# Performance work log

Measured on AMD Instinct MI355X. Metric: run time of the kernel, lower is better.

Reference implementation:

```python
import jax, jax.numpy as jnp
import numpy as np

# layer dims of the hard-coded linear chain (torch Linear: y = x @ W.T + b)
_DIMS = [784, 69, 31, 10, 10, 10, 10, 10, 10, 10]


def setup_inputs() -> dict:
    key = jax.random.key(0)
    ks = jax.random.split(key, 1 + 2 * 9)
    inp = {"x": jax.random.normal(ks[0], (65536, 784), dtype=jnp.float32)}
    for i in range(9):
        fan_in, fan_out = _DIMS[i], _DIMS[i + 1]
        bound = 1.0 / np.sqrt(fan_in)
        inp[f"W{i}"] = jax.random.uniform(ks[1 + 2 * i], (fan_out, fan_in), dtype=jnp.float32, minval=-bound, maxval=bound)
        inp[f"b{i}"] = jax.random.uniform(ks[2 + 2 * i], (fan_out,), dtype=jnp.float32, minval=-bound, maxval=bound)
    return inp


def reference(x, W0, b0, W1, b1, W2, b2, W3, b3, W4, b4, W5, b5, W6, b6, W7, b7, W8, b8):
    Ws = [W0, W1, W2, W3, W4, W5, W6, W7, W8]
    bs = [b0, b1, b2, b3, b4, b5, b6, b7, b8]
    for W, b in zip(Ws, bs):
        x = x @ W.T + b  # [B, out]
    return x
```

## Files before the change

### kernel.cpp

```cpp
#include <hip/hip_runtime.h>


__global__ void prep_all(
    const float* __restrict__ W0,
    const float* __restrict__ W1, const float* __restrict__ b1,
    const float* __restrict__ W2, const float* __restrict__ b2,
    const float* __restrict__ W3, const float* __restrict__ b3,
    const float* __restrict__ W4, const float* __restrict__ b4,
    const float* __restrict__ W5, const float* __restrict__ b5,
    const float* __restrict__ W6, const float* __restrict__ b6,
    const float* __restrict__ W7, const float* __restrict__ b7,
    const float* __restrict__ W8, const float* __restrict__ b8,
    const float* __restrict__ b0,
    float* __restrict__ Wt2, float* __restrict__ beff)
{
    __shared__ float Sa[31 * 69], Sb[31 * 69];
    __shared__ float da[31], db[31];
    const int t = threadIdx.x;
    const int nt = blockDim.x;

    for (int i = t; i < 31 * 69; i += nt) Sa[i] = W1[i];
    for (int i = t; i < 31; i += nt) da[i] = b1[i];
    __syncthreads();

    for (int i = t; i < 10 * 69; i += nt) {
        int o = i / 69, c = i - o * 69;
        float s = 0.f;
        for (int k = 0; k < 31; k++) s += W2[o * 31 + k] * Sa[k * 69 + c];
        Sb[i] = s;
    }
    for (int i = t; i < 10; i += nt) {
        float s = b2[i];
        for (int k = 0; k < 31; k++) s += W2[i * 31 + k] * da[k];
        db[i] = s;
    }
    __syncthreads();

    const float* Wk[6] = { W3, W4, W5, W6, W7, W8 };
    const float* bk[6] = { b3, b4, b5, b6, b7, b8 };
    int src = 1;
    for (int st = 0; st < 6; st++) {
        const float* W = Wk[st];
        const float* bb = bk[st];
        float* S  = src ? Sb : Sa;
        float* D  = src ? Sa : Sb;
        float* dd = src ? db : da;
        float* dn = src ? da : db;
        for (int i = t; i < 10 * 69; i += nt) {
            int o = i / 69, c = i - o * 69;
            float s = 0.f;
            for (int k = 0; k < 10; k++) s += W[o * 10 + k] * S[k * 69 + c];
            D[i] = s;
        }
        for (int i = t; i < 10; i += nt) {
            float s = bb[i];
            for (int k = 0; k < 10; k++) s += W[i * 10 + k] * dd[k];
            dn[i] = s;
        }
        __syncthreads();
        src ^= 1;
    }

    float* S  = src ? Sb : Sa;
    float* dd = src ? db : da;

    if (blockIdx.x == 0) {
        for (int i = t; i < 10; i += nt) {
            float s = dd[i];
            for (int k = 0; k < 69; k++) s += S[i * 69 + k] * b0[k];
            beff[i] = s;
        }
    }

    int e = blockIdx.x * nt + t;
    if (e < 8800) {
        int j4 = e / 44, rem = e - j4 * 44;
        float val = 0.f;
        if (rem < 40) {
            int o = rem >> 2, k = rem & 3, j = j4 * 4 + k;
            if (j < 784) {
                for (int u = 0; u < 69; u++) val += S[o * 69 + u] * W0[u * 784 + j];
            }
        }
        Wt2[e] = val;
    }
}


__global__ __launch_bounds__(512, 4) void linear_main(
    const float* __restrict__ x, const float* __restrict__ Wt2,
    const float* __restrict__ beff, float* __restrict__ out)
{
    __shared__ float4 wlds[2200];
    const int t = threadIdx.x;
    const int s = t & 7;
    const long row0 = (long)blockIdx.x * 128 + (t >> 3);
    const float* xr0 = x + row0 * 784;
    const float* xr1 = xr0 + (long)64 * 784;

    {
        const float4* wg = (const float4*)Wt2;
        for (int i = t; i < 2200; i += 512) wlds[i] = wg[i];
    }

    float acc0[10], acc1[10];
#pragma unroll
    for (int o = 0; o < 10; o++) { acc0[o] = 0.f; acc1[o] = 0.f; }

    float4 xv0 = *(const float4*)(xr0 + s * 4);
    float4 xv1 = *(const float4*)(xr1 + s * 4);
    __syncthreads();

    for (int jb = 0; jb < 25; jb++) {
        float4 xc0 = xv0, xc1 = xv1;
        if (jb < 24) {
            int jn = (jb + 1) * 32 + s * 4;
            jn = jn > 780 ? 780 : jn;
            xv0 = *(const float4*)(xr0 + jn);
            xv1 = *(const float4*)(xr1 + jn);
        }
        const float4* wrow = &wlds[(jb * 8 + s) * 11];
#pragma unroll
        for (int o = 0; o < 10; o++) {
            float4 wv = wrow[o];
            acc0[o] = fmaf(xc0.x, wv.x, acc0[o]);
            acc0[o] = fmaf(xc0.y, wv.y, acc0[o]);
            acc0[o] = fmaf(xc0.z, wv.z, acc0[o]);
            acc0[o] = fmaf(xc0.w, wv.w, acc0[o]);
            acc1[o] = fmaf(xc1.x, wv.x, acc1[o]);
            acc1[o] = fmaf(xc1.y, wv.y, acc1[o]);
            acc1[o] = fmaf(xc1.z, wv.z, acc1[o]);
            acc1[o] = fmaf(xc1.w, wv.w, acc1[o]);
        }
    }

#pragma unroll
    for (int m = 1; m < 8; m <<= 1)
#pragma unroll
        for (int o = 0; o < 10; o++) {
            acc0[o] += __shfl_xor(acc0[o], m, 64);
            acc1[o] += __shfl_xor(acc1[o], m, 64);
        }

    if (s < 5) {
        float lo0 = 0.f, hi0 = 0.f, lo1 = 0.f, hi1 = 0.f;
#pragma unroll
        for (int o = 0; o < 5; o++) {
            if (s == o) {
                lo0 = acc0[2 * o]; hi0 = acc0[2 * o + 1];
                lo1 = acc1[2 * o]; hi1 = acc1[2 * o + 1];
            }
        }
        float be0 = beff[s * 2], be1 = beff[s * 2 + 1];
        *(float2*)(out + row0 * 10 + s * 2) = make_float2(lo0 + be0, hi0 + be1);
        *(float2*)(out + (row0 + 64) * 10 + s * 2) = make_float2(lo1 + be0, hi1 + be1);
    }
}

extern "C" void kernel_launch(void* const* d_in, const int* in_sizes, int n_in,
                              void* d_out, int out_size, void* d_ws, size_t ws_size,
                              hipStream_t stream) {
    const float* x  = (const float*)d_in[0];
    const float* W0 = (const float*)d_in[1];
    const float* b0 = (const float*)d_in[2];
    const float* W1 = (const float*)d_in[3];
    const float* b1 = (const float*)d_in[4];
    const float* W2 = (const float*)d_in[5];
    const float* b2 = (const float*)d_in[6];
    const float* W3 = (const float*)d_in[7];
    const float* b3 = (const float*)d_in[8];
    const float* W4 = (const float*)d_in[9];
    const float* b4 = (const float*)d_in[10];
    const float* W5 = (const float*)d_in[11];
    const float* b5 = (const float*)d_in[12];
    const float* W6 = (const float*)d_in[13];
    const float* b6 = (const float*)d_in[14];
    const float* W7 = (const float*)d_in[15];
    const float* b7 = (const float*)d_in[16];
    const float* W8 = (const float*)d_in[17];
    const float* b8 = (const float*)d_in[18];

    float* ws   = (float*)d_ws;
    float* Wt2  = ws;
    float* beff = ws + 8800;

    float* out = (float*)d_out;
    const int B = in_sizes[0] / 784;

    prep_all<<<18, 512, 0, stream>>>(W0, W1, b1, W2, b2, W3, b3, W4, b4,
                                     W5, b5, W6, b6, W7, b7, W8, b8,
                                     b0, Wt2, beff);
    linear_main<<<B / 128, 512, 0, stream>>>(x, Wt2, beff, out);
}
```

Before: 335.9 us.

## Fuse weight-chain collapse into main kernel, recomputing per block

Removes the separate prep kernel and its global workspace round-trip. Each block now collapses W1..W8 and the bias chain in shared memory, then builds the 784x10 effective weight matrix directly into LDS before streaming x. This removes one launch and one dependency gap, but every one of the 512 blocks redoes the prep work, which costs about 0.5M FMAs plus W0 reads per block. Shared memory use also grows, which may reduce occupancy below the launch-bounds target.

Measured after the change: 364.2 us. 1.08x slower.

```diff
diff --git a/kernel.cpp b/kernel.cpp
--- a/kernel.cpp
+++ b/kernel.cpp
@@ -1,8 +1,9 @@
 #include <hip/hip_runtime.h>
 
 
-__global__ void prep_all(
-    const float* __restrict__ W0,
+__global__ __launch_bounds__(512, 4) void fused_main(
+    const float* __restrict__ x,
+    const float* __restrict__ W0, const float* __restrict__ b0,
     const float* __restrict__ W1, const float* __restrict__ b1,
     const float* __restrict__ W2, const float* __restrict__ b2,
     const float* __restrict__ W3, const float* __restrict__ b3,
@@ -11,28 +12,37 @@
     const float* __restrict__ W6, const float* __restrict__ b6,
     const float* __restrict__ W7, const float* __restrict__ b7,
     const float* __restrict__ W8, const float* __restrict__ b8,
-    const float* __restrict__ b0,
-    float* __restrict__ Wt2, float* __restrict__ beff)
+    float* __restrict__ out)
 {
+    __shared__ float4 wlds[2200];
     __shared__ float Sa[31 * 69], Sb[31 * 69];
-    __shared__ float da[31], db[31];
+    __shared__ float da[31], db[31], be[10];
+
     const int t = threadIdx.x;
-    const int nt = blockDim.x;
+    const int sseg = t & 7;
+    const long row0 = (long)blockIdx.x * 128 + (t >> 3);
+    const float* xr0 = x + row0 * 784;
+    const float* xr1 = xr0 + (long)64 * 784;
 
-    for (int i = t; i < 31 * 69; i += nt) Sa[i] = W1[i];
-    for (int i = t; i < 31; i += nt) da[i] = b1[i];
+    float4 xv0 = *(const float4*)(xr0 + sseg * 4);
+    float4 xv1 = *(const float4*)(xr1 + sseg * 4);
+
+    for (int i = t; i < 2200; i += 512) wlds[i] = make_float4(0.f, 0.f, 0.f, 0.f);
+
+    for (int i = t; i < 31 * 69; i += 512) Sa[i] = W1[i];
+    for (int i = t; i < 31; i += 512) da[i] = b1[i];
     __syncthreads();
 
-    for (int i = t; i < 10 * 69; i += nt) {
+    for (int i = t; i < 10 * 69; i += 512) {
         int o = i / 69, c = i - o * 69;
-        float s = 0.f;
-        for (int k = 0; k < 31; k++) s += W2[o * 31 + k] * Sa[k * 69 + c];
-        Sb[i] = s;
+        float v = 0.f;
+        for (int k = 0; k < 31; k++) v += W2[o * 31 + k] * Sa[k * 69 + c];
+        Sb[i] = v;
     }
-    for (int i = t; i < 10; i += nt) {
-        float s = b2[i];
-        for (int k = 0; k < 31; k++) s += W2[i * 31 + k] * da[k];
-        db[i] = s;
+    for (int i = t; i < 10; i += 512) {
+        float v = b2[i];
+        for (int k = 0; k < 31; k++) v += W2[i * 31 + k] * da[k];
+        db[i] = v;
     }
     __syncthreads();
 
@@ -46,16 +56,16 @@
         float* D  = src ? Sa : Sb;
         float* dd = src ? db : da;
         float* dn = src ? da : db;
-        for (int i = t; i < 10 * 69; i += nt) {
+        for (int i = t; i < 10 * 69; i += 512) {
             int o = i / 69, c = i - o * 69;
-            float s = 0.f;
-            for (int k = 0; k < 10; k++) s += W[o * 10 + k] * S[k * 69 + c];
-            D[i] = s;
+            float v = 0.f;
+            for (int k = 0; k < 10; k++) v += W[o * 10 + k] * S[k * 69 + c];
+            D[i] = v;
         }
-        for (int i = t; i < 10; i += nt) {
-            float s = bb[i];
-            for (int k = 0; k < 10; k++) s += W[i * 10 + k] * dd[k];
-            dn[i] = s;
+        for (int i = t; i < 10; i += 512) {
+            float v = bb[i];
+            for (int k = 0; k < 10; k++) v += W[i * 10 + k] * dd[k];
+            dn[i] = v;
         }
         __syncthreads();
         src ^= 1;
@@ -64,62 +74,57 @@
     float* S  = src ? Sb : Sa;
     float* dd = src ? db : da;
 
-    if (blockIdx.x == 0) {
-        for (int i = t; i < 10; i += nt) {
-            float s = dd[i];
-            for (int k = 0; k < 69; k++) s += S[i * 69 + k] * b0[k];
-            beff[i] = s;
+    for (int i = t; i < 10; i += 512) {
+        float v = dd[i];
+        for (int k = 0; k < 69; k++) v += S[i * 69 + k] * b0[k];
+        be[i] = v;
+    }
+
+    {
+        float a0[10], a1[10];
+#pragma unroll
+        for (int o = 0; o < 10; o++) { a0[o] = 0.f; a1[o] = 0.f; }
+        const bool two = (t < 272);
+        for (int u = 0; u < 69; u++) {
+            float s8v[10];
+#pragma unroll
+            for (int o = 0; o < 10; o++) s8v[o] = S[o * 69 + u];
+            float w0 = W0[u * 784 + t];
+#pragma unroll
+            for (int o = 0; o < 10; o++) a0[o] = fmaf(s8v[o], w0, a0[o]);
+            if (two) {
+                float w1 = W0[u * 784 + t + 512];
+#pragma unroll
+                for (int o = 0; o < 10; o++) a1[o] = fmaf(s8v[o], w1, a1[o]);
+            }
+        }
+        float* wf = (float*)wlds;
+        const int j = t;
+#pragma unroll
+        for (int o = 0; o < 10; o++)
+            wf[(j >> 2) * 44 + o * 4 + (j & 3)] = a0[o];
+        if (two) {
+            const int j2 = t + 512;
+#pragma unroll
+            for (int o = 0; o < 10; o++)
+                wf[(j2 >> 2) * 44 + o * 4 + (j2 & 3)] = a1[o];
         }
     }
-
-    int e = blockIdx.x * nt + t;
-    if (e < 8800) {
-        int j4 = e / 44, rem = e - j4 * 44;
-        float val = 0.f;
-        if (rem < 40) {
-            int o = rem >> 2, k = rem & 3, j = j4 * 4 + k;
-            if (j < 784) {
-                for (int u = 0; u < 69; u++) val += S[o * 69 + u] * W0[u * 784 + j];
-            }
-        }
-        Wt2[e] = val;
-    }
-}
-
-
-__global__ __launch_bounds__(512, 4) void linear_main(
-    const float* __restrict__ x, const float* __restrict__ Wt2,
-    const float* __restrict__ beff, float* __restrict__ out)
-{
-    __shared__ float4 wlds[2200];
-    const int t = threadIdx.x;
-    const int s = t & 7;
-    const long row0 = (long)blockIdx.x * 128 + (t >> 3);
-    const float* xr0 = x + row0 * 784;
-    const float* xr1 = xr0 + (long)64 * 784;
-
-    {
-        const float4* wg = (const float4*)Wt2;
-        for (int i = t; i < 2200; i += 512) wlds[i] = wg[i];
-    }
+    __syncthreads();
 
     float acc0[10], acc1[10];
 #pragma unroll
     for (int o = 0; o < 10; o++) { acc0[o] = 0.f; acc1[o] = 0.f; }
 
-    float4 xv0 = *(const float4*)(xr0 + s * 4);
-    float4 xv1 = *(const float4*)(xr1 + s * 4);
-    __syncthreads();
-
     for (int jb = 0; jb < 25; jb++) {
         float4 xc0 = xv0, xc1 = xv1;
         if (jb < 24) {
-            int jn = (jb + 1) * 32 + s * 4;
+            int jn = (jb + 1) * 32 + sseg * 4;
             jn = jn > 780 ? 780 : jn;
             xv0 = *(const float4*)(xr0 + jn);
             xv1 = *(const float4*)(xr1 + jn);
         }
-        const float4* wrow = &wlds[(jb * 8 + s) * 11];
+        const float4* wrow = &wlds[(jb * 8 + sseg) * 11];
 #pragma unroll
         for (int o = 0; o < 10; o++) {
             float4 wv = wrow[o];
@@ -142,18 +147,18 @@
             acc1[o] += __shfl_xor(acc1[o], m, 64);
         }
 
-    if (s < 5) {
+    if (sseg < 5) {
         float lo0 = 0.f, hi0 = 0.f, lo1 = 0.f, hi1 = 0.f;
 #pragma unroll
         for (int o = 0; o < 5; o++) {
-            if (s == o) {
+            if (sseg == o) {
                 lo0 = acc0[2 * o]; hi0 = acc0[2 * o + 1];
                 lo1 = acc1[2 * o]; hi1 = acc1[2 * o + 1];
             }
         }
-        float be0 = beff[s * 2], be1 = beff[s * 2 + 1];
-        *(float2*)(out + row0 * 10 + s * 2) = make_float2(lo0 + be0, hi0 + be1);
-        *(float2*)(out + (row0 + 64) * 10 + s * 2) = make_float2(lo1 + be0, hi1 + be1);
+        float be0 = be[sseg * 2], be1 = be[sseg * 2 + 1];
+        *(float2*)(out + row0 * 10 + sseg * 2) = make_float2(lo0 + be0, hi0 + be1);
+        *(float2*)(out + (row0 + 64) * 10 + sseg * 2) = make_float2(lo1 + be0, hi1 + be1);
     }
 }
 
@@ -179,16 +184,12 @@
     const float* b7 = (const float*)d_in[16];
     const float* W8 = (const float*)d_in[17];
     const float* b8 = (const float*)d_in[18];
-
-    float* ws   = (float*)d_ws;
-    float* Wt2  = ws;
-    float* beff = ws + 8800;
+    (void)d_ws; (void)ws_size;
 
     float* out = (float*)d_out;
     const int B = in_sizes[0] / 784;
 
-    prep_all<<<18, 512, 0, stream>>>(W0, W1, b1, W2, b2, W3, b3, W4, b4,
-                                     W5, b5, W6, b6, W7, b7, W8, b8,
-                                     b0, Wt2, beff);
-    linear_main<<<B / 128, 512, 0, stream>>>(x, Wt2, beff, out);
+    fused_main<<<B / 128, 512, 0, stream>>>(x,
+        W0, b0, W1, b1, W2, b2, W3, b3, W4, b4,
+        W5, b5, W6, b6, W7, b7, W8, b8, out);
 }
```
